# Kernel tuning notes

Measured on AMD Instinct MI355X. Metric: run time of the kernel, lower is better.

## Reference

```python
import jax, jax.numpy as jnp
import numpy as np

B = 1 << 20
N_FREQS = 6          # sin+cos -> 3*2*6 = 36 dims for position
N_BINS = 4           # one-blob bins -> 4 dims per scalar
W_SCALE = 0.18       # ~ sqrt(2/64) He init for ReLU


def freq_embed(p):
    # p: [B,3] -> [B, 3*2*N_FREQS] NeRF-style sin/cos frequency encoding
    freqs = (2.0 ** jnp.arange(N_FREQS, dtype=p.dtype)) * jnp.pi  # [F]
    ang = p[:, :, None] * freqs  # [B,3,F]
    return jnp.concatenate([jnp.sin(ang), jnp.cos(ang)], axis=-1).reshape(p.shape[0], -1)


def one_blob_embed(x):
    # x: [B,D] values in [0,1] -> [B, D*N_BINS] Gaussian one-blob encoding
    centers = (jnp.arange(N_BINS, dtype=x.dtype) + 0.5) / N_BINS  # [K]
    sigma = 1.0 / N_BINS
    val = jnp.exp(-0.5 * ((x[:, :, None] - centers) / sigma) ** 2)  # [B,D,K]
    return val.reshape(x.shape[0], -1)


def to_sphe_coords(d):
    # unit direction [B,3] -> normalized (theta, phi) in [0,1]^2
    theta = jnp.arccos(jnp.clip(d[:, 2], -1.0, 1.0)) / jnp.pi
    phi = jnp.arctan2(d[:, 1], d[:, 0]) / (2.0 * jnp.pi) + 0.5
    return jnp.stack([theta, phi], axis=-1)


def setup_inputs() -> dict:
    key = jax.random.key(0)
    ks = jax.random.split(key, 13)
    p = jax.random.normal(ks[0], (B, 3), dtype=jnp.float32)
    wi = jax.random.normal(ks[1], (B, 3), dtype=jnp.float32)
    wi = wi / jnp.linalg.norm(wi, axis=-1, keepdims=True)
    n = jax.random.normal(ks[2], (B, 3), dtype=jnp.float32)
    n = n / jnp.linalg.norm(n, axis=-1, keepdims=True)
    alpha = jax.random.uniform(ks[3], (B, 3), dtype=jnp.float32)
    beta = jax.random.uniform(ks[4], (B, 3), dtype=jnp.float32)
    r = jax.random.uniform(ks[5], (B, 1), dtype=jnp.float32)
    Ws = {}
    for i in range(6):
        Ws[f"W{i}"] = jax.random.normal(ks[6 + i], (64, 64), dtype=jnp.float32) * W_SCALE
    Ws["W6"] = jax.random.normal(ks[12], (3, 64), dtype=jnp.float32) * W_SCALE
    return dict(p=p, wi=wi, n=n, alpha=alpha, beta=beta, r=r, **Ws)


def reference(p, wi, n, alpha, beta, r, W0, W1, W2, W3, W4, W5, W6):
    x = jnp.concatenate([
        freq_embed(p),                               # 36
        one_blob_embed(to_sphe_coords(wi)),          # 8
        one_blob_embed(to_sphe_coords(n)),           # 8
        one_blob_embed(1.0 - jnp.exp(-r)),           # 4
        alpha,                                       # 3
        beta,                                        # 3
        jnp.ones_like(p[:, :2]),                     # 2 (implicit bias)
    ], axis=-1)  # [B,64]
    h = x
    for W in (W0, W1, W2, W3, W4, W5):
        h = jax.nn.relu(h @ W.T)
    out = h @ W6.T  # [B,3]
    return out * (alpha + beta)  # reflectance factorization
```

## Files before the change

kernel.cpp:

```cpp
#include <hip/hip_runtime.h>

typedef __attribute__((ext_vector_type(8))) short short8;
typedef __attribute__((ext_vector_type(4))) float f32x4;

typedef __attribute__((address_space(3))) unsigned short lds_us;
typedef const __attribute__((address_space(1))) unsigned short glb_us;

__device__ __forceinline__ unsigned short f2bf(float x) {
  union { float f; unsigned u; } v; v.f = x;
  unsigned r = v.u + 0x7fffu + ((v.u >> 16) & 1u);
  return (unsigned short)(r >> 16);
}

#if __has_builtin(__builtin_amdgcn_cvt_pk_bf16_f32)
__device__ __forceinline__ unsigned pk2(float a, float b) {
  return __builtin_bit_cast(unsigned, __builtin_amdgcn_cvt_pk_bf16_f32(a, b));
}
#else
__device__ __forceinline__ unsigned pk2(float a, float b) {
  union { float f; unsigned u; } x, y; x.f = a; y.f = b;
  return __builtin_amdgcn_perm(y.u + 0x8000u, x.u + 0x8000u, 0x07060302u);
}
#endif

__device__ __forceinline__ unsigned relu_pk(unsigned x) {
  unsigned r;
  asm("v_pk_max_i16 %0, %1, %2" : "=v"(r) : "v"(x), "v"(0));
  return r;
}

__device__ __forceinline__ short8 u2s8(uint4 u) {
  union { uint4 a; short8 b; } c; c.a = u; return c.b;
}

__device__ __forceinline__ void wave_mem_fence() {
  asm volatile("" ::: "memory");
  __builtin_amdgcn_wave_barrier();
  asm volatile("" ::: "memory");
}

__device__ __forceinline__ void gload16(const unsigned short* g, unsigned short* l) {
  __builtin_amdgcn_global_load_lds((glb_us*)g, (lds_us*)l, 16, 0, 0);
}

__device__ __forceinline__ float acos01(float z) {
  float ax = fminf(fabsf(z), 1.0f);
  float t  = __builtin_amdgcn_sqrtf(1.0f - ax);
  float p  = fmaf(ax, fmaf(ax, fmaf(ax, -0.00596110f, 0.02363618f),
                           -0.06751692f), 0.49998766f);
  p *= t;
  return z >= 0.0f ? p : 1.0f - p;
}

__device__ __forceinline__ float atan2_01(float y, float x) {
  float ax = fabsf(x), ay = fabsf(y);
  float hi = fmaxf(ax, ay), lo = fminf(ax, ay);
  float r  = lo * __builtin_amdgcn_rcpf(fmaxf(hi, 1e-30f));
  float r2 = r * r;
  float p  = fmaf(r2, fmaf(r2, fmaf(r2, fmaf(r2, fmaf(r2,
               -0.0018655370f, 0.0083800422f), -0.018531250f),
                0.030803547f), -0.052940457f), 0.159151323f);
  float q  = r * p;
  q = (ay > ax) ? 0.25f - q : q;
  q = (x < 0.0f) ? 0.5f - q : q;
  return 0.5f + ((y >= 0.0f) ? q : -q);
}

__device__ __forceinline__ uint2 blob4pk(float x) {
  float x4 = x * 4.0f;
  float e0, e1, e2, e3;
  { float t = x4 - 0.5f; e0 = __builtin_amdgcn_exp2f(t * t * -0.72134752f); }
  { float t = x4 - 1.5f; e1 = __builtin_amdgcn_exp2f(t * t * -0.72134752f); }
  { float t = x4 - 2.5f; e2 = __builtin_amdgcn_exp2f(t * t * -0.72134752f); }
  { float t = x4 - 3.5f; e3 = __builtin_amdgcn_exp2f(t * t * -0.72134752f); }
  return make_uint2(pk2(e0, e1), pk2(e2, e3));
}

__device__ __forceinline__ void freq6(float p, float* s, float* c) {
  float fr = __builtin_amdgcn_fractf(0.5f * p);
  float sv = __builtin_amdgcn_sinf(fr);
  float cv = __builtin_amdgcn_cosf(fr);
  s[0] = sv; c[0] = cv;
#pragma unroll
  for (int i = 1; i < 6; ++i) {
    float t  = sv * cv;
    float ss = sv * sv;
    sv = t + t;
    cv = 1.0f - (ss + ss);
    s[i] = sv; c[i] = cv;
  }
}

__global__ void prep_weights(
    const float* __restrict__ W0, const float* __restrict__ W1,
    const float* __restrict__ W2, const float* __restrict__ W3,
    const float* __restrict__ W4, const float* __restrict__ W5,
    const float* __restrict__ W6, unsigned short* __restrict__ wb)
{
  int idx = blockIdx.x * blockDim.x + threadIdx.x;
  if (idx < 24576) {
    int l = idx >> 12;
    const float* W = (l==0)?W0:(l==1)?W1:(l==2)?W2:(l==3)?W3:(l==4)?W4:W5;
    int j   = idx & 7;
    int ln  = (idx >> 3) & 63;
    int h   = (idx >> 9) & 1;
    int t   = (idx >> 10) & 3;
    int n15 = ln & 15, q = ln >> 4;
    int src = 32*(t>>1) + 8*(n15>>2) + 4*(t&1) + (n15&3);
    int col = h*32 + q*8 + j;
    wb[idx] = f2bf(W[src*64 + col]);
  } else if (idx < 25600) {
    int i6  = idx - 24576;
    int j   = i6 & 7;
    int ln  = (i6 >> 3) & 63;
    int h   = (i6 >> 9) & 1;
    int n15 = ln & 15, q = ln >> 4;
    wb[idx] = (n15 < 3) ? f2bf(W6[n15*64 + h*32 + q*8 + j]) : (unsigned short)0;
  }
}

__global__ __launch_bounds__(256, 3) void nrc_mlp(
    const float* __restrict__ P, const float* __restrict__ WI,
    const float* __restrict__ NRM, const float* __restrict__ ALPHA,
    const float* __restrict__ BETA, const float* __restrict__ R,
    const unsigned short* __restrict__ wb, float* __restrict__ out)
{
  __shared__ __align__(16) unsigned short lds[24576];
  const int lane = threadIdx.x & 63;
  const int wv   = threadIdx.x >> 6;
  const int n15  = lane & 15;
  const int q    = lane >> 4;
  const int l16  = lane * 8;
  unsigned short* Xw = lds + 8192 + (wv << 12);
  const int row0 = (blockIdx.x * 4 + wv) * 64;

  {
    int c0 = 2*wv*512;
    gload16(wb + c0 + l16,        lds + c0 + l16);
    gload16(wb + c0 + 512 + l16,  lds + c0 + 512 + l16);
  }

  {
    const int row = row0 + lane;
    const int sw  = lane & 7;
    unsigned short* xr = Xw + (lane << 6);
#define XST(j) (*(uint4*)(xr + (((j) ^ sw) << 3)))

    float s0[6], c0[6], s1[6], c1[6], s2[6], c2[6];
    freq6(P[row*3+0], s0, c0);
    freq6(P[row*3+1], s1, c1);
    freq6(P[row*3+2], s2, c2);

    XST(0) = make_uint4(pk2(s0[0],s0[1]), pk2(s0[2],s0[3]),
                        pk2(s0[4],s0[5]), pk2(c0[0],c0[1]));
    XST(1) = make_uint4(pk2(c0[2],c0[3]), pk2(c0[4],c0[5]),
                        pk2(s1[0],s1[1]), pk2(s1[2],s1[3]));
    XST(2) = make_uint4(pk2(s1[4],s1[5]), pk2(c1[0],c1[1]),
                        pk2(c1[2],c1[3]), pk2(c1[4],c1[5]));
    XST(3) = make_uint4(pk2(s2[0],s2[1]), pk2(s2[2],s2[3]),
                        pk2(s2[4],s2[5]), pk2(c2[0],c2[1]));

    uint2 bwt, bwp, bnt, bnp, brr;
    {
      float wx = WI[row*3+0], wy = WI[row*3+1], wz = WI[row*3+2];
      bwt = blob4pk(acos01(wz));
      bwp = blob4pk(atan2_01(wy, wx));
    }
    {
      float nx = NRM[row*3+0], ny = NRM[row*3+1], nz = NRM[row*3+2];
      bnt = blob4pk(acos01(nz));
      bnp = blob4pk(atan2_01(ny, nx));
    }
    brr = blob4pk(1.0f - __builtin_amdgcn_exp2f(R[row] * -1.44269504f));

    XST(4) = make_uint4(pk2(c2[2],c2[3]), pk2(c2[4],c2[5]), bwt.x, bwt.y);
    XST(5) = make_uint4(bwp.x, bwp.y, bnt.x, bnt.y);
    XST(6) = make_uint4(bnp.x, bnp.y, brr.x, brr.y);

    float a0 = ALPHA[row*3+0], a1 = ALPHA[row*3+1], a2 = ALPHA[row*3+2];
    float e0 = BETA[row*3+0],  e1 = BETA[row*3+1],  e2 = BETA[row*3+2];
    XST(7) = make_uint4(pk2(a0,a1), pk2(a2,e0), pk2(e1,e2), 0x3F803F80u);
#undef XST
  }
  wave_mem_fence();

  uint4 b0[4], b1[4];
  {
    const int swr = n15 & 7;
#pragma unroll
    for (int g = 0; g < 4; ++g) {
      const unsigned short* rb = Xw + ((g*16 + n15) << 6);
      b0[g] = *(const uint4*)(rb + (((q    ) ^ swr) << 3));
      b1[g] = *(const uint4*)(rb + (((q + 4) ^ swr) << 3));
    }
  }

  __syncthreads();

  const f32x4 z = {0.f, 0.f, 0.f, 0.f};

#pragma unroll
  for (int l = 0; l < 6; ++l) {
    if (l < 5) {
      unsigned short* nb = lds + ((l+1) & 1) * 4096;
      int ns = (l+1) * 4096;
      int c0 = 2*wv*512;
      gload16(wb + ns + c0 + l16,       nb + c0 + l16);
      gload16(wb + ns + c0 + 512 + l16, nb + c0 + 512 + l16);
    } else if (wv < 2) {
      int c0 = wv*512;
      gload16(wb + 24576 + c0 + l16, lds + c0 + l16);
    }

    const unsigned short* Wl = lds + (l & 1) * 4096;
    short8 a0[4], a1[4];
#pragma unroll
    for (int k = 0; k < 4; ++k) {
      a0[k] = *(const short8*)(Wl + k*1024 + l16);
      a1[k] = *(const short8*)(Wl + k*1024 + 512 + l16);
    }

    f32x4 acc[4][4];
#pragma unroll
    for (int k = 0; k < 4; ++k) {
#pragma unroll
      for (int g = 0; g < 4; ++g) {
        f32x4 c = __builtin_amdgcn_mfma_f32_16x16x32_bf16(a0[k], u2s8(b0[g]), z, 0, 0, 0);
        acc[g][k] = __builtin_amdgcn_mfma_f32_16x16x32_bf16(a1[k], u2s8(b1[g]), c, 0, 0, 0);
      }
    }

#pragma unroll
    for (int g = 0; g < 4; ++g) {
      uint4 n0, n1;
      n0.x = relu_pk(pk2(acc[g][0][0], acc[g][0][1]));
      n0.y = relu_pk(pk2(acc[g][0][2], acc[g][0][3]));
      n0.z = relu_pk(pk2(acc[g][1][0], acc[g][1][1]));
      n0.w = relu_pk(pk2(acc[g][1][2], acc[g][1][3]));
      n1.x = relu_pk(pk2(acc[g][2][0], acc[g][2][1]));
      n1.y = relu_pk(pk2(acc[g][2][2], acc[g][2][3]));
      n1.z = relu_pk(pk2(acc[g][3][0], acc[g][3][1]));
      n1.w = relu_pk(pk2(acc[g][3][2], acc[g][3][3]));
      b0[g] = n0; b1[g] = n1;
    }
    __syncthreads();
  }

  {
    short8 o0 = *(const short8*)(lds + l16);
    short8 o1 = *(const short8*)(lds + 512 + l16);
#pragma unroll
    for (int g = 0; g < 4; ++g) {
      f32x4 c = __builtin_amdgcn_mfma_f32_16x16x32_bf16(o0, u2s8(b0[g]), z, 0, 0, 0);
      c       = __builtin_amdgcn_mfma_f32_16x16x32_bf16(o1, u2s8(b1[g]), c, 0, 0, 0);
      if (q == 0) {
        int base = row0*3 + g*48 + n15*3;
        float3 av = *(const float3*)(ALPHA + base);
        float3 bv = *(const float3*)(BETA + base);
        float3 o;
        o.x = c[0] * (av.x + bv.x);
        o.y = c[1] * (av.y + bv.y);
        o.z = c[2] * (av.z + bv.z);
        *(float3*)(out + base) = o;
      }
    }
  }
}

extern "C" void kernel_launch(void* const* d_in, const int* in_sizes, int n_in,
                              void* d_out, int out_size, void* d_ws, size_t ws_size,
                              hipStream_t stream) {
  const float* P  = (const float*)d_in[0];
  const float* WI = (const float*)d_in[1];
  const float* NR = (const float*)d_in[2];
  const float* AL = (const float*)d_in[3];
  const float* BE = (const float*)d_in[4];
  const float* R  = (const float*)d_in[5];
  const float* W0 = (const float*)d_in[6];
  const float* W1 = (const float*)d_in[7];
  const float* W2 = (const float*)d_in[8];
  const float* W3 = (const float*)d_in[9];
  const float* W4 = (const float*)d_in[10];
  const float* W5 = (const float*)d_in[11];
  const float* W6 = (const float*)d_in[12];
  unsigned short* wb = (unsigned short*)d_ws;
  float* out = (float*)d_out;

  prep_weights<<<100, 256, 0, stream>>>(W0, W1, W2, W3, W4, W5, W6, wb);
  nrc_mlp<<<4096, 256, 0, stream>>>(P, WI, NR, AL, BE, R, wb, out);
}
```

Measured before the change: 164.2 us.

## Load MLP weights directly from global into registers, drop LDS staging and barriers

Weight fragments for each layer are now read directly from global memory (L1/L2 cached) into a register double buffer instead of staged through LDS with global_load_lds. This removes the block-wide __syncthreads per layer and shrinks shared memory, which may raise occupancy. In exchange every wave issues its own global loads for the same weights, and register pressure rises from holding two sets of eight weight fragments.

```diff
diff --git a/kernel.cpp b/kernel.cpp
--- a/kernel.cpp
+++ b/kernel.cpp
@@ -2,9 +2,6 @@
 
 typedef __attribute__((ext_vector_type(8))) short short8;
 typedef __attribute__((ext_vector_type(4))) float f32x4;
-
-typedef __attribute__((address_space(3))) unsigned short lds_us;
-typedef const __attribute__((address_space(1))) unsigned short glb_us;
 
 __device__ __forceinline__ unsigned short f2bf(float x) {
   union { float f; unsigned u; } v; v.f = x;
@@ -37,10 +34,6 @@
   asm volatile("" ::: "memory");
   __builtin_amdgcn_wave_barrier();
   asm volatile("" ::: "memory");
-}
-
-__device__ __forceinline__ void gload16(const unsigned short* g, unsigned short* l) {
-  __builtin_amdgcn_global_load_lds((glb_us*)g, (lds_us*)l, 16, 0, 0);
 }
 
 __device__ __forceinline__ float acos01(float z) {
@@ -125,19 +118,20 @@
     const float* __restrict__ BETA, const float* __restrict__ R,
     const unsigned short* __restrict__ wb, float* __restrict__ out)
 {
-  __shared__ __align__(16) unsigned short lds[24576];
+  __shared__ __align__(16) unsigned short lds[16384];
   const int lane = threadIdx.x & 63;
   const int wv   = threadIdx.x >> 6;
   const int n15  = lane & 15;
   const int q    = lane >> 4;
   const int l16  = lane * 8;
-  unsigned short* Xw = lds + 8192 + (wv << 12);
+  unsigned short* Xw = lds + (wv << 12);
   const int row0 = (blockIdx.x * 4 + wv) * 64;
 
-  {
-    int c0 = 2*wv*512;
-    gload16(wb + c0 + l16,        lds + c0 + l16);
-    gload16(wb + c0 + 512 + l16,  lds + c0 + 512 + l16);
+  short8 aa[2][8];
+#pragma unroll
+  for (int k = 0; k < 4; ++k) {
+    aa[0][k]   = *(const short8*)(wb + k*1024 + l16);
+    aa[0][4+k] = *(const short8*)(wb + k*1024 + 512 + l16);
   }
 
   {
@@ -195,38 +189,31 @@
     }
   }
 
-  __syncthreads();
-
   const f32x4 z = {0.f, 0.f, 0.f, 0.f};
 
 #pragma unroll
   for (int l = 0; l < 6; ++l) {
+    const int cur = l & 1, nxt = cur ^ 1;
+
     if (l < 5) {
-      unsigned short* nb = lds + ((l+1) & 1) * 4096;
-      int ns = (l+1) * 4096;
-      int c0 = 2*wv*512;
-      gload16(wb + ns + c0 + l16,       nb + c0 + l16);
-      gload16(wb + ns + c0 + 512 + l16, nb + c0 + 512 + l16);
-    } else if (wv < 2) {
-      int c0 = wv*512;
-      gload16(wb + 24576 + c0 + l16, lds + c0 + l16);
-    }
-
-    const unsigned short* Wl = lds + (l & 1) * 4096;
-    short8 a0[4], a1[4];
+      const unsigned short* wn = wb + (l+1)*4096 + l16;
+#pragma unroll
+      for (int k = 0; k < 4; ++k) {
+        aa[nxt][k]   = *(const short8*)(wn + k*1024);
+        aa[nxt][4+k] = *(const short8*)(wn + k*1024 + 512);
+      }
+    } else {
+      aa[nxt][0] = *(const short8*)(wb + 24576 + l16);
+      aa[nxt][1] = *(const short8*)(wb + 24576 + 512 + l16);
+    }
+
+    f32x4 acc[4][4];
 #pragma unroll
     for (int k = 0; k < 4; ++k) {
-      a0[k] = *(const short8*)(Wl + k*1024 + l16);
-      a1[k] = *(const short8*)(Wl + k*1024 + 512 + l16);
-    }
-
-    f32x4 acc[4][4];
-#pragma unroll
-    for (int k = 0; k < 4; ++k) {
 #pragma unroll
       for (int g = 0; g < 4; ++g) {
-        f32x4 c = __builtin_amdgcn_mfma_f32_16x16x32_bf16(a0[k], u2s8(b0[g]), z, 0, 0, 0);
-        acc[g][k] = __builtin_amdgcn_mfma_f32_16x16x32_bf16(a1[k], u2s8(b1[g]), c, 0, 0, 0);
+        f32x4 c = __builtin_amdgcn_mfma_f32_16x16x32_bf16(aa[cur][k], u2s8(b0[g]), z, 0, 0, 0);
+        acc[g][k] = __builtin_amdgcn_mfma_f32_16x16x32_bf16(aa[cur][4+k], u2s8(b1[g]), c, 0, 0, 0);
       }
     }
 
@@ -243,12 +230,11 @@
       n1.w = relu_pk(pk2(acc[g][3][2], acc[g][3][3]));
       b0[g] = n0; b1[g] = n1;
     }
-    __syncthreads();
   }
 
   {
-    short8 o0 = *(const short8*)(lds + l16);
-    short8 o1 = *(const short8*)(lds + 512 + l16);
+    short8 o0 = aa[0][0];
+    short8 o1 = aa[0][1];
 #pragma unroll
     for (int g = 0; g < 4; ++g) {
       f32x4 c = __builtin_amdgcn_mfma_f32_16x16x32_bf16(o0, u2s8(b0[g]), z, 0, 0, 0);
```

Measured after the change: 162.9 us. Within noise of the previous version (-0.8%).
